# Performance work log

Measured on AMD Instinct MI355X. Metric: run time of the kernel, lower is better.

## Reference

```python
import jax, jax.numpy as jnp
import numpy as np
import math

D, NH, HD, L, P = 256, 8, 32, 4, 4
SS = np.array([[128, 128], [64, 64], [32, 32], [16, 16]], dtype=np.int32)   # (H, W) per level
LSI = np.array([0, 16384, 20480, 21504], dtype=np.int32)
N_TOTAL, B, Q = 21760, 8, 1000


def setup_inputs() -> dict:
    key = jax.random.key(0)
    ks = jax.random.split(key, 10)
    s = 0.02
    # directional bias as in the torch init (cos/sin per head, tiled over levels/points)
    thetas = jnp.arange(NH, dtype=jnp.float32) * (2.0 * math.pi / NH)
    grid = jnp.stack([jnp.cos(thetas), jnp.sin(thetas)], axis=-1)            # [NH,2]
    b_off = jnp.broadcast_to(grid[:, None, None, :], (NH, L, P, 2)).reshape(-1)
    return {
        'query': jax.random.normal(ks[0], (Q, B, D), jnp.float32),
        'reference_points': jax.random.uniform(ks[1], (Q, B, 2), jnp.float32),
        'value': jax.random.normal(ks[2], (N_TOTAL, B, D), jnp.float32),
        'spatial_shapes': jnp.asarray(SS),
        'level_start_idx': jnp.asarray(LSI),
        'W_v': jax.random.normal(ks[3], (D, D), jnp.float32) * s,
        'b_v': jnp.zeros((D,), jnp.float32),
        'W_off': jax.random.normal(ks[4], (D, NH * L * P * 2), jnp.float32) * s,
        'b_off': b_off,
        'W_attn': jax.random.normal(ks[5], (D, NH * L * P), jnp.float32) * s,
        'b_attn': jnp.zeros((NH * L * P,), jnp.float32),
        'W_out': jax.random.normal(ks[6], (D, D), jnp.float32) * s,
        'b_out': jnp.zeros((D,), jnp.float32),
    }


def _msda_forward(query, reference_points, value, ss, lsi,
                  W_v, b_v, W_off, b_off, W_attn, b_attn, W_out, b_out):
    Qn, Bn, _ = query.shape
    # value projection -> [B, N, NH, HD]
    v = (value @ W_v + b_v).transpose(1, 0, 2).reshape(Bn, -1, NH, HD)
    q = query.transpose(1, 0, 2)                                             # [B,Q,D]
    off = (q @ W_off + b_off).reshape(Bn, Qn, NH, L, P, 2)
    aw = jax.nn.softmax((q @ W_attn + b_attn).reshape(Bn, Qn, NH, L * P), axis=-1)
    aw = aw.reshape(Bn, Qn, NH, L, P)
    ref = reference_points.transpose(1, 0, 2)                                # [B,Q,2]
    ss_f = ss.astype(np.float32)
    norm = np.stack([ss_f[:, 1], ss_f[:, 0]], axis=-1)                       # (W,H) per level, [L,2]
    loc = ref[:, :, None, None, None, :] + off / (jnp.asarray(norm)[None, None, None, :, None, :] + 1e-6)
    loc = jnp.clip(loc, 0.0, 1.0)                                            # [B,Q,NH,L,P,2]

    bi = jnp.arange(Bn)[:, None, None, None]
    hi = jnp.arange(NH)[None, None, :, None]
    out = jnp.zeros((Bn, Qn, NH, HD), query.dtype)
    for lvl in range(L):
        H, W = int(ss[lvl, 0]), int(ss[lvl, 1])
        start = int(lsi[lvl])
        vf = v[:, start:start + H * W].transpose(0, 2, 1, 3)                 # [B,NH,H*W,HD]
        g = loc[:, :, :, lvl] * 2.0 - 1.0                                    # [B,Q,NH,P,2]
        # grid_sample align_corners=False pixel coords
        x = (g[..., 0] + 1.0) * (W * 0.5) - 0.5
        y = (g[..., 1] + 1.0) * (H * 0.5) - 0.5
        x0 = jnp.floor(x); y0 = jnp.floor(y)
        wx1 = x - x0; wy1 = y - y0
        x0i = x0.astype(jnp.int32); y0i = y0.astype(jnp.int32)
        samp = jnp.zeros(x.shape + (HD,), query.dtype)
        for dx, wx in ((0, 1.0 - wx1), (1, wx1)):
            for dy, wy in ((0, 1.0 - wy1), (1, wy1)):
                xi = x0i + dx; yi = y0i + dy
                valid = (xi >= 0) & (xi < W) & (yi >= 0) & (yi < H)          # zero padding
                idx = jnp.clip(yi, 0, H - 1) * W + jnp.clip(xi, 0, W - 1)
                corner = vf[bi, hi, idx]                                     # [B,Q,NH,P,HD]
                samp = samp + corner * (wx * wy * valid)[..., None]
        out = out + (samp * aw[:, :, :, lvl, :, None]).sum(axis=3)
    out = out.reshape(Bn, Qn, D) @ W_out + b_out
    return out.transpose(1, 0, 2)                                            # [Q,B,D]


def reference(query, reference_points, value, spatial_shapes, level_start_idx,
              W_v, b_v, W_off, b_off, W_attn, b_attn, W_out, b_out):
    ss = np.asarray(jax.device_get(spatial_shapes))
    lsi = np.asarray(jax.device_get(level_start_idx))
    return _msda_forward(query, reference_points, value, ss, lsi,
                         W_v, b_v, W_off, b_off, W_attn, b_attn, W_out, b_out)
```

## Files before the change

### kernel.cpp

```cpp
#include <hip/hip_runtime.h>
#include <math.h>

#define QQ     1000
#define BBATCH 8
#define NTOT   21760

typedef __bf16 bf16x8 __attribute__((ext_vector_type(8)));
typedef float  f32x4  __attribute__((ext_vector_type(4)));

__device__ __forceinline__ unsigned short bf_hi(float f, float* rem) {
    unsigned u = __builtin_bit_cast(unsigned, f);
    unsigned r = (u + 0x7FFFu + ((u >> 16) & 1u)) >> 16;
    float hf = __builtin_bit_cast(float, r << 16);
    *rem = f - hf;
    return (unsigned short)r;
}
__device__ __forceinline__ unsigned short bf_rn(float f) {
    unsigned u = __builtin_bit_cast(unsigned, f);
    return (unsigned short)((u + 0x7FFFu + ((u >> 16) & 1u)) >> 16);
}

__global__ __launch_bounds__(256) void conv_wv(
    const float* __restrict__ Wv,
    unsigned short* __restrict__ Bh, unsigned short* __restrict__ Bl)
{
    const int tid = threadIdx.x;
    const int n   = blockIdx.x * 8 + (tid >> 5);
    const int oct = tid & 31;
    const int k0  = oct * 8;
    float r0, r1, r2, r3, r4, r5, r6, r7;
    const unsigned h0 = bf_hi(Wv[(k0+0)*256 + n], &r0);
    const unsigned h1 = bf_hi(Wv[(k0+1)*256 + n], &r1);
    const unsigned h2 = bf_hi(Wv[(k0+2)*256 + n], &r2);
    const unsigned h3 = bf_hi(Wv[(k0+3)*256 + n], &r3);
    const unsigned h4 = bf_hi(Wv[(k0+4)*256 + n], &r4);
    const unsigned h5 = bf_hi(Wv[(k0+5)*256 + n], &r5);
    const unsigned h6 = bf_hi(Wv[(k0+6)*256 + n], &r6);
    const unsigned h7 = bf_hi(Wv[(k0+7)*256 + n], &r7);
    uint4 hv, lv;
    hv.x = h0 | (h1 << 16); hv.y = h2 | (h3 << 16);
    hv.z = h4 | (h5 << 16); hv.w = h6 | (h7 << 16);
    lv.x = (unsigned)bf_rn(r0) | ((unsigned)bf_rn(r1) << 16);
    lv.y = (unsigned)bf_rn(r2) | ((unsigned)bf_rn(r3) << 16);
    lv.z = (unsigned)bf_rn(r4) | ((unsigned)bf_rn(r5) << 16);
    lv.w = (unsigned)bf_rn(r6) | ((unsigned)bf_rn(r7) << 16);
    const int c  = oct >> 3;
    const int sp = (oct & 7) ^ (n & 7);
    const size_t byte = (size_t)n * 512 + (size_t)c * 128 + (size_t)sp * 16;
    *reinterpret_cast<uint4*>((char*)Bh + byte) = hv;
    *reinterpret_cast<uint4*>((char*)Bl + byte) = lv;
}

__global__ __launch_bounds__(256) void conv_wcat(
    const float* __restrict__ W_off, const float* __restrict__ W_attn,
    const float* __restrict__ W_out,
    unsigned short* __restrict__ Bh, unsigned short* __restrict__ Bl)
{
    const int tid = threadIdx.x;
    const int n   = blockIdx.x * 8 + (tid >> 5);
    const int oct = tid & 31;
    const int k0  = oct * 8;
    const float* src; int col, ld;
    if (n < 256)      { src = W_off;  col = n;       ld = 256; }
    else if (n < 384) { src = W_attn; col = n - 256; ld = 128; }
    else              { src = W_out;  col = n - 384; ld = 256; }
    unsigned hw[8], lw[8];
#pragma unroll
    for (int j = 0; j < 8; ++j) {
        float r;
        hw[j] = bf_hi(src[(size_t)(k0 + j) * ld + col], &r);
        lw[j] = bf_rn(r);
    }
    uint4 hv, lv;
    hv.x = hw[0] | (hw[1] << 16); hv.y = hw[2] | (hw[3] << 16);
    hv.z = hw[4] | (hw[5] << 16); hv.w = hw[6] | (hw[7] << 16);
    lv.x = lw[0] | (lw[1] << 16); lv.y = lw[2] | (lw[3] << 16);
    lv.z = lw[4] | (lw[5] << 16); lv.w = lw[6] | (lw[7] << 16);
    const int c  = oct >> 3;
    const int sp = (oct & 7) ^ (n & 7);
    const size_t byte = (size_t)n * 512 + (size_t)c * 128 + (size_t)sp * 16;
    *reinterpret_cast<uint4*>((char*)Bh + byte) = hv;
    *reinterpret_cast<uint4*>((char*)Bl + byte) = lv;
}

__global__ __launch_bounds__(256, 2) void gemm_value_mfma(
    const float* __restrict__ A,
    const unsigned short* __restrict__ Bth, const unsigned short* __restrict__ Btl,
    const float* __restrict__ bias, float* __restrict__ C)
{
    __shared__ unsigned short Ah_lds[64 * 64];
    __shared__ unsigned short Al_lds[64 * 64];
    __shared__ unsigned short Bh_lds[256 * 64];
    __shared__ unsigned short Bl_lds[256 * 64];

    const int tid  = threadIdx.x;
    const int lane = tid & 63;
    const int w    = tid >> 6;
    const int m0   = blockIdx.x * 64;

    f32x4 acc[4][4];
#pragma unroll
    for (int i = 0; i < 4; ++i)
#pragma unroll
        for (int j = 0; j < 4; ++j) acc[i][j] = (f32x4){0.f, 0.f, 0.f, 0.f};

    for (int kc = 0; kc < 256; kc += 64) {
        __syncthreads();
#pragma unroll
        for (int u = 0; u < 4; ++u) {
            const int idx = tid + u * 256;
            const int row = idx >> 4;
            const int c4  = (idx & 15) * 4;
            const float4 av = *reinterpret_cast<const float4*>(
                &A[(size_t)(m0 + row) * 256 + kc + c4]);
            float r0, r1, r2, r3;
            const unsigned e0 = bf_hi(av.x, &r0);
            const unsigned e1 = bf_hi(av.y, &r1);
            const unsigned e2 = bf_hi(av.z, &r2);
            const unsigned e3 = bf_hi(av.w, &r3);
            uint2 hp, lp;
            hp.x = e0 | (e1 << 16);
            hp.y = e2 | (e3 << 16);
            lp.x = (unsigned)bf_rn(r0) | ((unsigned)bf_rn(r1) << 16);
            lp.y = (unsigned)bf_rn(r2) | ((unsigned)bf_rn(r3) << 16);
            const unsigned byte = (unsigned)(row * 128 + c4 * 2) ^ ((unsigned)(row & 7) << 4);
            *reinterpret_cast<uint2*>((char*)Ah_lds + byte) = hp;
            *reinterpret_cast<uint2*>((char*)Al_lds + byte) = lp;
        }
        {
            const int r8 = lane >> 3, sl = lane & 7;
#pragma unroll
            for (int i = 0; i < 16; ++i) {
                const int chunk = w * 16 + i;
                const int plane = chunk >> 5;
                const int crow  = (chunk & 31) * 8;
                const unsigned short* gb = plane ? Btl : Bth;
                const size_t gbyte = (size_t)(crow + r8) * 512 + (size_t)kc * 2 + (size_t)sl * 16;
                unsigned short* lbase = (plane ? Bl_lds : Bh_lds) + crow * 64;
                __builtin_amdgcn_global_load_lds(
                    (const __attribute__((address_space(1))) void*)((const char*)gb + gbyte),
                    (__attribute__((address_space(3))) void*)lbase,
                    16, 0, 0);
            }
        }
        __syncthreads();
#pragma unroll
        for (int kk = 0; kk < 2; ++kk) {
            bf16x8 ah[4], al[4], bh[4], bl[4];
            const int slot = kk * 4 + (lane >> 4);
#pragma unroll
            for (int fr = 0; fr < 4; ++fr) {
                const int row = fr * 16 + (lane & 15);
                const unsigned byte = (unsigned)(row * 128) + ((unsigned)(slot ^ (row & 7)) << 4);
                ah[fr] = *reinterpret_cast<const bf16x8*>((const char*)Ah_lds + byte);
                al[fr] = *reinterpret_cast<const bf16x8*>((const char*)Al_lds + byte);
            }
#pragma unroll
            for (int fc = 0; fc < 4; ++fc) {
                const int n = w * 64 + fc * 16 + (lane & 15);
                const unsigned byte = (unsigned)(n * 128) + ((unsigned)(slot ^ (n & 7)) << 4);
                bh[fc] = *reinterpret_cast<const bf16x8*>((const char*)Bh_lds + byte);
                bl[fc] = *reinterpret_cast<const bf16x8*>((const char*)Bl_lds + byte);
            }
#pragma unroll
            for (int fr = 0; fr < 4; ++fr)
#pragma unroll
                for (int fc = 0; fc < 4; ++fc) {
                    acc[fr][fc] = __builtin_amdgcn_mfma_f32_16x16x32_bf16(ah[fr], bh[fc], acc[fr][fc], 0, 0, 0);
                    acc[fr][fc] = __builtin_amdgcn_mfma_f32_16x16x32_bf16(al[fr], bh[fc], acc[fr][fc], 0, 0, 0);
                    acc[fr][fc] = __builtin_amdgcn_mfma_f32_16x16x32_bf16(ah[fr], bl[fc], acc[fr][fc], 0, 0, 0);
                }
        }
    }
#pragma unroll
    for (int fc = 0; fc < 4; ++fc) {
        const int col = w * 64 + fc * 16 + (lane & 15);
        const float bv = bias[col];
#pragma unroll
        for (int fr = 0; fr < 4; ++fr)
#pragma unroll
            for (int ri = 0; ri < 4; ++ri) {
                const int gr = m0 + fr * 16 + (lane >> 4) * 4 + ri;
                const int orow = (gr & 7) * NTOT + (gr >> 3);
                C[(size_t)orow * 256 + col] = acc[fr][fc][ri] + bv;
            }
    }
}

template<int MODE>
__global__ __launch_bounds__(256, 2) void gemm_q_mfma(
    const float* __restrict__ A,
    const unsigned short* __restrict__ Bth, const unsigned short* __restrict__ Btl,
    const float* __restrict__ bias0, const float* __restrict__ bias1,
    float* __restrict__ C0, float* __restrict__ C1,
    const int N, const int rmod, const int rmul)
{
    __shared__ unsigned short Ah_lds[64 * 64];
    __shared__ unsigned short Al_lds[64 * 64];
    __shared__ unsigned short Bh_lds[256 * 64];
    __shared__ unsigned short Bl_lds[256 * 64];

    const int tid  = threadIdx.x;
    const int lane = tid & 63;
    const int w    = tid >> 6;
    const int m0   = blockIdx.x * 64;
    const int n0   = blockIdx.y * 256;
    const int ac   = min(256, N - n0);
    const bool active = (w * 64) < ac;
    const int cpw  = ac >> 4;
    const int rpp  = ac >> 3;

    f32x4 acc[4][4];
#pragma unroll
    for (int i = 0; i < 4; ++i)
#pragma unroll
        for (int j = 0; j < 4; ++j) acc[i][j] = (f32x4){0.f, 0.f, 0.f, 0.f};

    for (int kc = 0; kc < 256; kc += 64) {
        __syncthreads();
#pragma unroll
        for (int u = 0; u < 4; ++u) {
            const int idx = tid + u * 256;
            const int row = idx >> 4;
            const int c4  = (idx & 15) * 4;
            const float4 av = *reinterpret_cast<const float4*>(
                &A[(size_t)(m0 + row) * 256 + kc + c4]);
            float r0, r1, r2, r3;
            const unsigned e0 = bf_hi(av.x, &r0);
            const unsigned e1 = bf_hi(av.y, &r1);
            const unsigned e2 = bf_hi(av.z, &r2);
            const unsigned e3 = bf_hi(av.w, &r3);
            uint2 hp, lp;
            hp.x = e0 | (e1 << 16);
            hp.y = e2 | (e3 << 16);
            lp.x = (unsigned)bf_rn(r0) | ((unsigned)bf_rn(r1) << 16);
            lp.y = (unsigned)bf_rn(r2) | ((unsigned)bf_rn(r3) << 16);
            const unsigned byte = (unsigned)(row * 128 + c4 * 2) ^ ((unsigned)(row & 7) << 4);
            *reinterpret_cast<uint2*>((char*)Ah_lds + byte) = hp;
            *reinterpret_cast<uint2*>((char*)Al_lds + byte) = lp;
        }
        {
            const int r8 = lane >> 3, sl = lane & 7;
            for (int i = 0; i < cpw; ++i) {
                const int chunk = w * cpw + i;
                const int plane = chunk >= rpp;
                const int crow  = (plane ? chunk - rpp : chunk) * 8;
                const unsigned short* gb = plane ? Btl : Bth;
                const size_t gbyte = (size_t)(n0 + crow + r8) * 512 + (size_t)kc * 2 + (size_t)sl * 16;
                unsigned short* lbase = (plane ? Bl_lds : Bh_lds) + crow * 64;
                __builtin_amdgcn_global_load_lds(
                    (const __attribute__((address_space(1))) void*)((const char*)gb + gbyte),
                    (__attribute__((address_space(3))) void*)lbase,
                    16, 0, 0);
            }
        }
        __syncthreads();
        if (active) {
#pragma unroll
            for (int kk = 0; kk < 2; ++kk) {
                bf16x8 ah[4], al[4], bh[4], bl[4];
                const int slot = kk * 4 + (lane >> 4);
#pragma unroll
                for (int fr = 0; fr < 4; ++fr) {
                    const int row = fr * 16 + (lane & 15);
                    const unsigned byte = (unsigned)(row * 128) + ((unsigned)(slot ^ (row & 7)) << 4);
                    ah[fr] = *reinterpret_cast<const bf16x8*>((const char*)Ah_lds + byte);
                    al[fr] = *reinterpret_cast<const bf16x8*>((const char*)Al_lds + byte);
                }
#pragma unroll
                for (int fc = 0; fc < 4; ++fc) {
                    const int n = w * 64 + fc * 16 + (lane & 15);
                    const unsigned byte = (unsigned)(n * 128) + ((unsigned)(slot ^ (n & 7)) << 4);
                    bh[fc] = *reinterpret_cast<const bf16x8*>((const char*)Bh_lds + byte);
                    bl[fc] = *reinterpret_cast<const bf16x8*>((const char*)Bl_lds + byte);
                }
#pragma unroll
                for (int fr = 0; fr < 4; ++fr)
#pragma unroll
                    for (int fc = 0; fc < 4; ++fc) {
                        acc[fr][fc] = __builtin_amdgcn_mfma_f32_16x16x32_bf16(ah[fr], bh[fc], acc[fr][fc], 0, 0, 0);
                        acc[fr][fc] = __builtin_amdgcn_mfma_f32_16x16x32_bf16(al[fr], bh[fc], acc[fr][fc], 0, 0, 0);
                        acc[fr][fc] = __builtin_amdgcn_mfma_f32_16x16x32_bf16(ah[fr], bl[fc], acc[fr][fc], 0, 0, 0);
                    }
            }
        }
    }
    if (!active) return;
#pragma unroll
    for (int fc = 0; fc < 4; ++fc) {
        const int colg = n0 + w * 64 + fc * 16 + (lane & 15);
#pragma unroll
        for (int fr = 0; fr < 4; ++fr)
#pragma unroll
            for (int ri = 0; ri < 4; ++ri) {
                const int gr = m0 + fr * 16 + (lane >> 4) * 4 + ri;
                const float v = acc[fr][fc][ri];
                if (MODE == 0) {
                    const int orow = (gr % rmod) * rmul + gr / rmod;
                    C0[(size_t)orow * 256 + colg] = v + bias0[colg];
                } else {
                    if (colg < 256) C0[(size_t)gr * 256 + colg] = v + bias0[colg];
                    else            C1[(size_t)gr * 128 + colg - 256] = v + bias1[colg - 256];
                }
            }
    }
}

__global__ __launch_bounds__(256) void msda_sample(
    const float* __restrict__ vproj, const float* __restrict__ off_raw,
    const float* __restrict__ attn_raw, const float* __restrict__ refp,
    float* __restrict__ tmp)
{
    const int lane = threadIdx.x & 63;
    const int widx = blockIdx.x * 4 + (threadIdx.x >> 6);
    const int h  = widx & 7;
    const int bq = widx >> 3;
    const int b  = bq / QQ;
    const int qi = bq - b * QQ;
    const int row_q = qi * BBATCH + b;

    const int s0 = lane & 15;
    const int l0 = s0 >> 2;
    float a = attn_raw[row_q * 128 + h * 16 + s0];
    float m = a;
#pragma unroll
    for (int msk = 8; msk >= 1; msk >>= 1) m = fmaxf(m, __shfl_xor(m, msk));
    const float e = __expf(a - m);
    float ssum = e;
#pragma unroll
    for (int msk = 8; msk >= 1; msk >>= 1) ssum += __shfl_xor(ssum, msk);
    const float wv = e / ssum;

    const float offx = off_raw[row_q * 256 + (h * 16 + s0) * 2 + 0];
    const float offy = off_raw[row_q * 256 + (h * 16 + s0) * 2 + 1];
    const float rx = refp[row_q * 2 + 0];
    const float ry = refp[row_q * 2 + 1];
    const float Wf = (float)(128 >> l0);
    float lx = rx + offx / (Wf + 1e-6f);
    float ly = ry + offy / (Wf + 1e-6f);
    lx = fminf(fmaxf(lx, 0.f), 1.f);
    ly = fminf(fmaxf(ly, 0.f), 1.f);
    const float xv = lx * Wf - 0.5f;
    const float yv = ly * Wf - 0.5f;

    const int c = lane & 31;
    const int sbase = (lane >> 5) * 8;
    const float* __restrict__ vb = vproj + (size_t)b * NTOT * 256 + h * 32 + c;

    float acc = 0.f;
#pragma unroll
    for (int i = 0; i < 8; ++i) {
        const int s = sbase + i;
        const float xs = __shfl(xv, s);
        const float ys = __shfl(yv, s);
        const float ws = __shfl(wv, s);
        const int l = s >> 2;
        const int Wl = 128 >> l;
        const int start = (65536 - (65536 >> (2 * l))) / 3;
        const float x0f = floorf(xs), y0f = floorf(ys);
        const float fx = xs - x0f, fy = ys - y0f;
        const int x0 = (int)x0f, y0 = (int)y0f;
        const int x1 = x0 + 1,   y1 = y0 + 1;
        const float vx0 = (x0 >= 0 && x0 < Wl) ? 1.f : 0.f;
        const float vx1 = (x1 >= 0 && x1 < Wl) ? 1.f : 0.f;
        const float vy0 = (y0 >= 0 && y0 < Wl) ? 1.f : 0.f;
        const float vy1 = (y1 >= 0 && y1 < Wl) ? 1.f : 0.f;
        const int xc0 = min(max(x0, 0), Wl - 1);
        const int xc1 = min(max(x1, 0), Wl - 1);
        const int yc0 = min(max(y0, 0), Wl - 1);
        const int yc1 = min(max(y1, 0), Wl - 1);
        const float* base = vb + (size_t)start * 256;
        const float v00 = base[(size_t)(yc0 * Wl + xc0) * 256];
        const float v10 = base[(size_t)(yc0 * Wl + xc1) * 256];
        const float v01 = base[(size_t)(yc1 * Wl + xc0) * 256];
        const float v11 = base[(size_t)(yc1 * Wl + xc1) * 256];
        const float w00 = (1.f - fx) * (1.f - fy) * vx0 * vy0;
        const float w10 = fx * (1.f - fy) * vx1 * vy0;
        const float w01 = (1.f - fx) * fy * vx0 * vy1;
        const float w11 = fx * fy * vx1 * vy1;
        acc += ws * (w00 * v00 + w10 * v10 + w01 * v01 + w11 * v11);
    }
    acc += __shfl_xor(acc, 32);
    if (lane < 32) tmp[(size_t)bq * 256 + h * 32 + c] = acc;
}

extern "C" void kernel_launch(void* const* d_in, const int* in_sizes, int n_in,
                              void* d_out, int out_size, void* d_ws, size_t ws_size,
                              hipStream_t stream) {
    (void)in_sizes; (void)n_in; (void)out_size; (void)ws_size;

    const float* query  = (const float*)d_in[0];
    const float* refp   = (const float*)d_in[1];
    const float* value  = (const float*)d_in[2];
    const float* W_v    = (const float*)d_in[5];
    const float* b_v    = (const float*)d_in[6];
    const float* W_off  = (const float*)d_in[7];
    const float* b_off  = (const float*)d_in[8];
    const float* W_attn = (const float*)d_in[9];
    const float* b_attn = (const float*)d_in[10];
    const float* W_out  = (const float*)d_in[11];
    const float* b_out  = (const float*)d_in[12];
    float* out = (float*)d_out;

    float* vproj    = (float*)d_ws;
    float* off_raw  = vproj + (size_t)44564480;
    float* attn_raw = off_raw + 2048000;
    float* tmp      = attn_raw + 1024000;
    unsigned short* Bt_h   = (unsigned short*)tmp;
    unsigned short* Bt_l   = Bt_h + 65536;
    unsigned short* Wcat_h = (unsigned short*)(tmp + 2048000);
    unsigned short* Wcat_l = Wcat_h + 640 * 256;

    const dim3 blk(256);
    conv_wv<<<dim3(32), blk, 0, stream>>>(W_v, Bt_h, Bt_l);
    conv_wcat<<<dim3(80), blk, 0, stream>>>(W_off, W_attn, W_out, Wcat_h, Wcat_l);
    gemm_value_mfma<<<dim3(2720), blk, 0, stream>>>(value, Bt_h, Bt_l, b_v, vproj);
    gemm_q_mfma<1><<<dim3(125, 2), blk, 0, stream>>>(
        query, Wcat_h, Wcat_l, b_off, b_attn, off_raw, attn_raw, 384, 0, 0);
    msda_sample<<<dim3(16000), blk, 0, stream>>>(vproj, off_raw, attn_raw, refp, tmp);
    gemm_q_mfma<0><<<dim3(125, 1), blk, 0, stream>>>(
        tmp, Wcat_h + 384 * 256, Wcat_l + 384 * 256, b_out, nullptr,
        out, nullptr, 256, 1000, 8);
}
```

Before: 433.2 us.

## Split value GEMM over N tiles and vectorize sampling gathers per corner

The value-projection GEMM now uses 64x128 tiles over a 2D grid instead of 64x256 tiles. This halves LDS and accumulator use so three blocks can share a CU, at the cost of converting each A tile to bf16 hi/lo twice. The sampling kernel now gives each lane one bilinear corner and four channels, loading float4 values and reducing across lanes with shuffles, in place of four scalar gathers per lane. This aims at more coalesced wide loads and fewer address computations, but adds a three-step shuffle reduction.

```diff
diff --git a/kernel.cpp b/kernel.cpp
--- a/kernel.cpp
+++ b/kernel.cpp
@@ -83,26 +83,27 @@
     *reinterpret_cast<uint4*>((char*)Bl + byte) = lv;
 }
 
-__global__ __launch_bounds__(256, 2) void gemm_value_mfma(
+__global__ __launch_bounds__(256, 3) void gemm_value_mfma(
     const float* __restrict__ A,
     const unsigned short* __restrict__ Bth, const unsigned short* __restrict__ Btl,
     const float* __restrict__ bias, float* __restrict__ C)
 {
     __shared__ unsigned short Ah_lds[64 * 64];
     __shared__ unsigned short Al_lds[64 * 64];
-    __shared__ unsigned short Bh_lds[256 * 64];
-    __shared__ unsigned short Bl_lds[256 * 64];
+    __shared__ unsigned short Bh_lds[128 * 64];
+    __shared__ unsigned short Bl_lds[128 * 64];
 
     const int tid  = threadIdx.x;
     const int lane = tid & 63;
     const int w    = tid >> 6;
     const int m0   = blockIdx.x * 64;
-
-    f32x4 acc[4][4];
+    const int n0   = blockIdx.y * 128;
+
+    f32x4 acc[4][2];
 #pragma unroll
     for (int i = 0; i < 4; ++i)
 #pragma unroll
-        for (int j = 0; j < 4; ++j) acc[i][j] = (f32x4){0.f, 0.f, 0.f, 0.f};
+        for (int j = 0; j < 2; ++j) acc[i][j] = (f32x4){0.f, 0.f, 0.f, 0.f};
 
     for (int kc = 0; kc < 256; kc += 64) {
         __syncthreads();
@@ -130,12 +131,12 @@
         {
             const int r8 = lane >> 3, sl = lane & 7;
 #pragma unroll
-            for (int i = 0; i < 16; ++i) {
-                const int chunk = w * 16 + i;
-                const int plane = chunk >> 5;
-                const int crow  = (chunk & 31) * 8;
+            for (int i = 0; i < 8; ++i) {
+                const int chunk = w * 8 + i;
+                const int plane = chunk >> 4;
+                const int crow  = (chunk & 15) * 8;
                 const unsigned short* gb = plane ? Btl : Bth;
-                const size_t gbyte = (size_t)(crow + r8) * 512 + (size_t)kc * 2 + (size_t)sl * 16;
+                const size_t gbyte = (size_t)(n0 + crow + r8) * 512 + (size_t)kc * 2 + (size_t)sl * 16;
                 unsigned short* lbase = (plane ? Bl_lds : Bh_lds) + crow * 64;
                 __builtin_amdgcn_global_load_lds(
                     (const __attribute__((address_space(1))) void*)((const char*)gb + gbyte),
@@ -146,7 +147,7 @@
         __syncthreads();
 #pragma unroll
         for (int kk = 0; kk < 2; ++kk) {
-            bf16x8 ah[4], al[4], bh[4], bl[4];
+            bf16x8 ah[4], al[4], bh[2], bl[2];
             const int slot = kk * 4 + (lane >> 4);
 #pragma unroll
             for (int fr = 0; fr < 4; ++fr) {
@@ -156,8 +157,8 @@
                 al[fr] = *reinterpret_cast<const bf16x8*>((const char*)Al_lds + byte);
             }
 #pragma unroll
-            for (int fc = 0; fc < 4; ++fc) {
-                const int n = w * 64 + fc * 16 + (lane & 15);
+            for (int fc = 0; fc < 2; ++fc) {
+                const int n = w * 32 + fc * 16 + (lane & 15);
                 const unsigned byte = (unsigned)(n * 128) + ((unsigned)(slot ^ (n & 7)) << 4);
                 bh[fc] = *reinterpret_cast<const bf16x8*>((const char*)Bh_lds + byte);
                 bl[fc] = *reinterpret_cast<const bf16x8*>((const char*)Bl_lds + byte);
@@ -165,7 +166,7 @@
 #pragma unroll
             for (int fr = 0; fr < 4; ++fr)
 #pragma unroll
-                for (int fc = 0; fc < 4; ++fc) {
+                for (int fc = 0; fc < 2; ++fc) {
                     acc[fr][fc] = __builtin_amdgcn_mfma_f32_16x16x32_bf16(ah[fr], bh[fc], acc[fr][fc], 0, 0, 0);
                     acc[fr][fc] = __builtin_amdgcn_mfma_f32_16x16x32_bf16(al[fr], bh[fc], acc[fr][fc], 0, 0, 0);
                     acc[fr][fc] = __builtin_amdgcn_mfma_f32_16x16x32_bf16(ah[fr], bl[fc], acc[fr][fc], 0, 0, 0);
@@ -173,8 +174,8 @@
         }
     }
 #pragma unroll
-    for (int fc = 0; fc < 4; ++fc) {
-        const int col = w * 64 + fc * 16 + (lane & 15);
+    for (int fc = 0; fc < 2; ++fc) {
+        const int col = n0 + w * 32 + fc * 16 + (lane & 15);
         const float bv = bias[col];
 #pragma unroll
         for (int fr = 0; fr < 4; ++fr)
@@ -343,14 +344,16 @@
     const float xv = lx * Wf - 0.5f;
     const float yv = ly * Wf - 0.5f;
 
-    const int c = lane & 31;
-    const int sbase = (lane >> 5) * 8;
-    const float* __restrict__ vb = vproj + (size_t)b * NTOT * 256 + h * 32 + c;
-
-    float acc = 0.f;
+    const int half   = lane >> 5;
+    const int corner = (lane >> 3) & 3;
+    const int c4     = lane & 7;
+    const int dx = corner & 1, dy = corner >> 1;
+    const float* __restrict__ vb = vproj + (size_t)b * NTOT * 256 + h * 32 + c4 * 4;
+
+    f32x4 pacc = (f32x4){0.f, 0.f, 0.f, 0.f};
 #pragma unroll
     for (int i = 0; i < 8; ++i) {
-        const int s = sbase + i;
+        const int s = i * 2 + half;
         const float xs = __shfl(xv, s);
         const float ys = __shfl(yv, s);
         const float ws = __shfl(wv, s);
@@ -359,29 +362,30 @@
         const int start = (65536 - (65536 >> (2 * l))) / 3;
         const float x0f = floorf(xs), y0f = floorf(ys);
         const float fx = xs - x0f, fy = ys - y0f;
-        const int x0 = (int)x0f, y0 = (int)y0f;
-        const int x1 = x0 + 1,   y1 = y0 + 1;
-        const float vx0 = (x0 >= 0 && x0 < Wl) ? 1.f : 0.f;
-        const float vx1 = (x1 >= 0 && x1 < Wl) ? 1.f : 0.f;
-        const float vy0 = (y0 >= 0 && y0 < Wl) ? 1.f : 0.f;
-        const float vy1 = (y1 >= 0 && y1 < Wl) ? 1.f : 0.f;
-        const int xc0 = min(max(x0, 0), Wl - 1);
-        const int xc1 = min(max(x1, 0), Wl - 1);
-        const int yc0 = min(max(y0, 0), Wl - 1);
-        const int yc1 = min(max(y1, 0), Wl - 1);
-        const float* base = vb + (size_t)start * 256;
-        const float v00 = base[(size_t)(yc0 * Wl + xc0) * 256];
-        const float v10 = base[(size_t)(yc0 * Wl + xc1) * 256];
-        const float v01 = base[(size_t)(yc1 * Wl + xc0) * 256];
-        const float v11 = base[(size_t)(yc1 * Wl + xc1) * 256];
-        const float w00 = (1.f - fx) * (1.f - fy) * vx0 * vy0;
-        const float w10 = fx * (1.f - fy) * vx1 * vy0;
-        const float w01 = (1.f - fx) * fy * vx0 * vy1;
-        const float w11 = fx * fy * vx1 * vy1;
-        acc += ws * (w00 * v00 + w10 * v10 + w01 * v01 + w11 * v11);
-    }
-    acc += __shfl_xor(acc, 32);
-    if (lane < 32) tmp[(size_t)bq * 256 + h * 32 + c] = acc;
+        const int xi = (int)x0f + dx;
+        const int yi = (int)y0f + dy;
+        const bool ok = (xi >= 0) && (xi < Wl) && (yi >= 0) && (yi < Wl);
+        const int xc = min(max(xi, 0), Wl - 1);
+        const int yc = min(max(yi, 0), Wl - 1);
+        const float wc = (dx ? fx : 1.f - fx) * (dy ? fy : 1.f - fy) * (ok ? ws : 0.f);
+        const float4 v4 = *reinterpret_cast<const float4*>(
+            vb + (size_t)(start + yc * Wl + xc) * 256);
+        pacc[0] += wc * v4.x;
+        pacc[1] += wc * v4.y;
+        pacc[2] += wc * v4.z;
+        pacc[3] += wc * v4.w;
+    }
+#pragma unroll
+    for (int msk = 8; msk <= 32; msk <<= 1) {
+        pacc[0] += __shfl_xor(pacc[0], msk);
+        pacc[1] += __shfl_xor(pacc[1], msk);
+        pacc[2] += __shfl_xor(pacc[2], msk);
+        pacc[3] += __shfl_xor(pacc[3], msk);
+    }
+    if (lane < 8) {
+        float4 o; o.x = pacc[0]; o.y = pacc[1]; o.z = pacc[2]; o.w = pacc[3];
+        *reinterpret_cast<float4*>(&tmp[(size_t)bq * 256 + h * 32 + lane * 4]) = o;
+    }
 }
 
 extern "C" void kernel_launch(void* const* d_in, const int* in_sizes, int n_in,
@@ -414,7 +418,7 @@
     const dim3 blk(256);
     conv_wv<<<dim3(32), blk, 0, stream>>>(W_v, Bt_h, Bt_l);
     conv_wcat<<<dim3(80), blk, 0, stream>>>(W_off, W_attn, W_out, Wcat_h, Wcat_l);
-    gemm_value_mfma<<<dim3(2720), blk, 0, stream>>>(value, Bt_h, Bt_l, b_v, vproj);
+    gemm_value_mfma<<<dim3(2720, 2), blk, 0, stream>>>(value, Bt_h, Bt_l, b_v, vproj);
     gemm_q_mfma<1><<<dim3(125, 2), blk, 0, stream>>>(
         query, Wcat_h, Wcat_l, b_off, b_attn, off_raw, attn_raw, 384, 0, 0);
     msda_sample<<<dim3(16000), blk, 0, stream>>>(vproj, off_raw, attn_raw, refp, tmp);
```

New measurement: 424.6 us. -2.0%, faster.
